# Performance work log

Hardware: AMD Instinct MI355X
Metric: run time of the kernel (lower is better)

Reference implementation:

```python
import jax, jax.numpy as jnp
import numpy as np

NUM_CLASSES = 80
ALPHA = 0.25
GAMMA = 2.0
CONF_T = 0.5
IOU_T = 0.5
N_ANCHORS = 6144


def _pairwise_iou(b):
    # b: [n,4] (x1,y1,x2,y2) -> [n,n] IoU matrix
    area = (b[:, 2] - b[:, 0]) * (b[:, 3] - b[:, 1])
    lt = jnp.maximum(b[:, None, :2], b[None, :, :2])
    rb = jnp.minimum(b[:, None, 2:], b[None, :, 2:])
    wh = jnp.clip(rb - lt, 0.0)
    inter = wh[..., 0] * wh[..., 1]
    return inter / (area[:, None] + area[None, :] - inter)


def _nms(boxes, scores, thr):
    # torchvision-style NMS: returns kept indices in decreasing-score order
    order = jnp.argsort(-scores)
    iou = _pairwise_iou(boxes[order])
    n = boxes.shape[0]
    ar = jnp.arange(n)
    def body(i, supp):
        return supp | ((iou[i] > thr) & (ar > i) & jnp.logical_not(supp[i]))
    supp = jax.lax.fori_loop(0, n, body, jnp.zeros(n, dtype=bool))
    kept_pos = jnp.where(~supp)[0]  # eager: concrete shapes
    return order[kept_pos]


def _make_boxes(tb, floc):
    # tb: [1,1,4] target box; floc: [Nf,2] filtered predicted locations
    # replicates loc_determined with T=1: (tx1*px, ty1*py, tx2*px, ty2*py)
    px, py = floc[:, 0], floc[:, 1]
    return jnp.stack([tb[0, 0, 0] * px, tb[0, 0, 1] * py,
                      tb[0, 0, 2] * px, tb[0, 0, 3] * py], axis=1)


def _smooth_l1_sum(pred, tgt):
    d = jnp.abs(pred - tgt)  # broadcasts [k,C,4] vs [1,1,4]
    return jnp.where(d < 1.0, 0.5 * d * d, d - 0.5).sum()


def setup_inputs() -> dict:
    key = jax.random.key(0)
    k1, k2, k3 = jax.random.split(key, 3)
    locations = jax.random.uniform(k1, (1, N_ANCHORS, 2), dtype=jnp.float32)
    confidences = jax.random.uniform(k2, (1, N_ANCHORS, NUM_CLASSES), dtype=jnp.float32)
    # valid target box (x1<x2, y1<y2) in [0,1]
    target_boxes = jnp.array([[[0.15, 0.2, 0.85, 0.9]]], dtype=jnp.float32)
    target_labels = jax.random.randint(k3, (1,), 0, NUM_CLASSES)
    return {"locations": locations, "confidences": confidences,
            "target_boxes": target_boxes, "target_labels": target_labels}


def reference(locations, confidences, target_boxes, target_labels):
    conf = confidences[0]                       # [N,C]
    scores_max = conf.max(axis=1)
    idx_f = jnp.where(scores_max > CONF_T)[0]   # eager boolean filter
    if idx_f.shape[0] == 0:
        return jnp.float32(0.001)
    floc = locations[0, idx_f, :]               # [Nf,2]
    fconf = conf[idx_f]                         # [Nf,C]
    boxes = _make_boxes(target_boxes, floc)     # [Nf,4] (pred_loc_final)
    score = fconf[:, 0]                         # class-0 score, as in original
    keep = _nms(boxes, score, IOU_T)            # kept indices
    if keep.shape[0] == 0:
        return jnp.float32(0.001)
    matched_loc = boxes[keep]                   # [M,4]
    matched_conf = fconf[keep]                  # [M,C]
    k = target_labels.shape[0]                  # = 1
    topv, topi = jax.lax.top_k(matched_conf.T, k)  # per-class top-k over dim 0
    topv, topi = topv.T, topi.T                 # [k,C]
    pred_bin = (topv[:, 0] > 0.5).astype(jnp.float32)  # [k]
    mloc = matched_loc[topi]                    # [k,C,4]
    loc_loss = _smooth_l1_sum(mloc, target_boxes)
    # F.cross_entropy with 1-D float input/target = probabilities mode, unbatched
    ce = -(target_labels.astype(jnp.float32) * jax.nn.log_softmax(pred_bin)).sum()
    focal = ALPHA * (1.0 - jnp.exp(-ce)) ** GAMMA * ce
    # original bug preserved: num_positives = sum of kept *indices*
    num_pos = keep.sum().astype(jnp.float32)
    return (loc_loss + focal) / num_pos
```

## Files before the change

### kernel.cpp

```cpp
#include <hip/hip_runtime.h>
#include <stdint.h>

#define N_ANCHORS 6144
#define NUM_CLASSES 80
#define NWORDS 96
#define NTILES 24
#define SCAN_B 32

__device__ unsigned long long g_mask[(size_t)N_ANCHORS * NWORDS + 64];
__device__ float4 g_sbox[N_ANCHORS];
__device__ int    g_rpart[NTILES][N_ANCHORS];
__device__ int    g_fpart[NTILES][N_ANCHORS];
__device__ int    g_sAnchor[N_ANCHORS];
__device__ int    g_sFi[N_ANCHORS];
__device__ int    g_keptPos[N_ANCHORS];
__device__ int    g_F, g_K, g_np, g_done;
__device__ float  g_loss;

__device__ __forceinline__ float rdlf(float v, int l) {
    return __int_as_float(__builtin_amdgcn_readlane(__float_as_int(v), l));
}

__device__ __forceinline__ float anchor_key(const float* __restrict__ conf, int i, bool& valid) {
    const float4* cp4 = (const float4*)(conf + (size_t)i * NUM_CLASSES);
    float4 v0 = cp4[0];
    float score = v0.x;
    float m = fmaxf(fmaxf(v0.x, v0.y), fmaxf(v0.z, v0.w));
    #pragma unroll
    for (int c = 1; c < NUM_CLASSES / 4; ++c) {
        float4 v = cp4[c];
        m = fmaxf(m, fmaxf(fmaxf(v.x, v.y), fmaxf(v.z, v.w)));
    }
    valid = m > 0.5f;
    return valid ? score : -1.0f;
}

__global__ void __launch_bounds__(256) k_rank(const float* __restrict__ conf) {
    __shared__ float skey[256];
    int y = blockIdx.y;
    int j0 = y * 256;
    bool vj;
    skey[threadIdx.x] = anchor_key(conf, j0 + threadIdx.x, vj);
    int i = blockIdx.x * 256 + threadIdx.x;
    bool vi;
    float ki = anchor_key(conf, i, vi);
    __syncthreads();
    int r = 0, f = 0;
    #pragma unroll 8
    for (int jj = 0; jj < 256; ++jj) {
        float kj = skey[jj];
        int j = j0 + jj;
        bool valid_j = kj >= 0.0f;
        r += (kj > ki) || (kj == ki && j < i && valid_j);
        f += (j < i) && valid_j;
    }
    g_rpart[y][i] = r;
    g_fpart[y][i] = f;
}

__global__ void __launch_bounds__(256) k_scatter(const float* __restrict__ loc,
                                                 const float* __restrict__ conf,
                                                 const float* __restrict__ tb) {
    int i = blockIdx.x * 256 + threadIdx.x;
    bool vi;
    float ki = anchor_key(conf, i, vi);
    (void)ki;
    int r = 0, f = 0;
    #pragma unroll
    for (int y = 0; y < NTILES; ++y) { r += g_rpart[y][i]; f += g_fpart[y][i]; }
    if (vi) {
        float px = loc[2 * i], py = loc[2 * i + 1];
        float4 b;
        b.x = __fmul_rn(tb[0], px);
        b.y = __fmul_rn(tb[1], py);
        b.z = __fmul_rn(tb[2], px);
        b.w = __fmul_rn(tb[3], py);
        g_sbox[r] = b;
        g_sAnchor[r] = i;
        g_sFi[r] = f;
    }
    if (i == N_ANCHORS - 1) g_F = f + (vi ? 1 : 0);
}

__global__ void __launch_bounds__(256) k_mask(void) {
    int wave = (blockIdx.x * 256 + threadIdx.x) >> 6;
    int lane = threadIdx.x & 63;
    if (wave >= N_ANCHORS) return;
    int i = wave;
    float4 bi = g_sbox[i];
    float areai = __fmul_rn(bi.z - bi.x, bi.w - bi.y);
    unsigned long long* row = g_mask + (size_t)i * NWORDS;
    for (int w = (i >> 6); w < NWORDS; ++w) {
        float4 bj = g_sbox[w * 64 + lane];
        float areaj = __fmul_rn(bj.z - bj.x, bj.w - bj.y);
        float lx = fmaxf(bi.x, bj.x), ly = fmaxf(bi.y, bj.y);
        float rx = fminf(bi.z, bj.z), ry = fminf(bi.w, bj.w);
        float iw = fmaxf(rx - lx, 0.0f), ih = fmaxf(ry - ly, 0.0f);
        float inter = __fmul_rn(iw, ih);
        float denom = __fsub_rn(__fadd_rn(areai, areaj), inter);
        float iou = __fdiv_rn(inter, denom);
        unsigned long long bits = __ballot(iou > 0.5f);
        if (lane == 0) row[w] = bits;
    }
}

__global__ void __launch_bounds__(64, 1) k_scan(void) {
    __shared__ int slots[SCAN_B];
    int lane = threadIdx.x;
    int F = g_F;
    if (lane == 0) { g_loss = 0.0f; g_np = 0; g_done = 0; }
    if (lane < SCAN_B) slots[lane] = 0;
    auto initw = [&](int w) -> unsigned long long {
        long long lo = (long long)w * 64, hi = lo + 64;
        if (F <= lo) return ~0ull;
        if (F >= hi) return 0ull;
        return (~0ull) << (F - lo);
    };
    unsigned long long remv0 = initw(lane);
    unsigned long long remv1 = (lane < 32) ? initw(64 + lane) : ~0ull;
    unsigned long long kept0 = 0, kept1 = 0;
    int lastPos = -1;

    while (true) {
        unsigned long long c0 = ~remv0;
        unsigned long long c1 = (lane < 32) ? ~remv1 : 0ull;
        {
            long long lo = (long long)lane << 6;
            if (lastPos >= lo + 63)      c0 = 0ull;
            else if (lastPos >= lo)      c0 &= (~0ull) << (int)(lastPos - lo + 1);
        }
        if (lane < 32) {
            long long lo = (long long)(64 + lane) << 6;
            if (lastPos >= lo + 63)      c1 = 0ull;
            else if (lastPos >= lo)      c1 &= (~0ull) << (int)(lastPos - lo + 1);
        }
        int n0 = __popcll(c0), n1 = __popcll(c1);
        int xp = (n0 << 16) | n1;
        for (int ofs = 1; ofs < 64; ofs <<= 1) {
            int y = __shfl_up(xp, ofs, 64);
            if (lane >= ofs) xp += y;
        }
        int lastxp = __builtin_amdgcn_readlane(xp, 63);
        int tot0 = lastxp >> 16, tot1 = lastxp & 0xffff;
        int total = tot0 + tot1;
        if (total == 0) break;
        int nb = (total < SCAN_B) ? total : SCAN_B;
        int off0 = (xp >> 16) - n0;
        int off1 = tot0 + ((xp & 0xffff) - n1);
        {
            unsigned long long wd = c0; int r = off0;
            while (wd && r < SCAN_B) { int b = __builtin_ctzll(wd); slots[r++] = lane * 64 + b; wd &= wd - 1; }
        }
        if (lane < 32) {
            unsigned long long wd = c1; int r = off1;
            while (wd && r < SCAN_B) { int b = __builtin_ctzll(wd); slots[r++] = (64 + lane) * 64 + b; wd &= wd - 1; }
        }
        __syncthreads();
        int myPos = slots[lane & 31];

        int Ps[SCAN_B];
        unsigned long long r0[SCAN_B], r1[SCAN_B];
        #pragma unroll
        for (int p = 0; p < SCAN_B; ++p) {
            Ps[p] = __builtin_amdgcn_readlane(myPos, p);
            const unsigned long long* rp = g_mask + (size_t)Ps[p] * NWORDS;
            r0[p] = rp[lane];
            r1[p] = rp[64 + lane];
        }

        float4 bj = g_sbox[myPos];
        float areaj = __fmul_rn(bj.z - bj.x, bj.w - bj.y);

        uint32_t conflict = 0;
        #pragma unroll
        for (int p = 0; p < SCAN_B; ++p) {
            float bix = rdlf(bj.x, p), biy = rdlf(bj.y, p), biz = rdlf(bj.z, p), biw = rdlf(bj.w, p);
            float areai = __fmul_rn(biz - bix, biw - biy);
            float lx = fmaxf(bix, bj.x), ly = fmaxf(biy, bj.y);
            float rx = fminf(biz, bj.z), ry = fminf(biw, bj.w);
            float iw = fmaxf(rx - lx, 0.0f), ih = fmaxf(ry - ly, 0.0f);
            float inter = __fmul_rn(iw, ih);
            float denom = __fsub_rn(__fadd_rn(areai, areaj), inter);
            float iou = __fdiv_rn(inter, denom);
            if (iou > 0.5f) conflict |= 1u << p;
        }
        conflict &= (nb >= 32) ? 0xffffffffu : ((1u << nb) - 1u);
        conflict &= (lane < nb) ? ((1u << lane) - 1u) : 0u;

        uint32_t keptm = 0;
        for (int p = 0; p < nb; ++p) {
            uint32_t cp = (uint32_t)__builtin_amdgcn_readlane((int)conflict, p);
            if ((cp & keptm) == 0u) keptm |= 1u << p;
        }

        #pragma unroll
        for (int p = 0; p < SCAN_B; ++p) {
            if ((keptm >> p) & 1u) {
                remv0 |= r0[p];
                remv1 |= r1[p];
                int P = Ps[p];
                int w = P >> 6, b = P & 63;
                if (w < 64) { if (lane == w) kept0 |= 1ull << b; }
                else        { if (lane == w - 64) kept1 |= 1ull << b; }
            }
        }
        lastPos = __builtin_amdgcn_readlane(myPos, nb - 1);
    }

    int c0 = __popcll(kept0);
    int c1 = (lane < 32) ? __popcll(kept1) : 0;
    int xp = (c0 << 16) | c1;
    for (int ofs = 1; ofs < 64; ofs <<= 1) {
        int y = __shfl_up(xp, ofs, 64);
        if (lane >= ofs) xp += y;
    }
    int lastxp = __builtin_amdgcn_readlane(xp, 63);
    int t0 = lastxp >> 16, t1 = lastxp & 0xffff;
    int off = (xp >> 16) - c0;
    unsigned long long wd = kept0;
    while (wd) { int b = __builtin_ctzll(wd); g_keptPos[off++] = lane * 64 + b; wd &= wd - 1; }
    off = t0 + ((xp & 0xffff) - c1);
    wd = kept1;
    while (wd) { int b = __builtin_ctzll(wd); g_keptPos[off++] = (64 + lane) * 64 + b; wd &= wd - 1; }
    if (lane == 0) g_K = t0 + t1;
}

__global__ void __launch_bounds__(64) k_loss(const float* __restrict__ conf, const float* __restrict__ tb,
                                             float* __restrict__ out) {
    int c = blockIdx.x;
    int lane = threadIdx.x;
    int K = g_K;
    float bv = -3.402823466e+38f;
    int bk = 0x7fffffff;
    int np = 0;
    for (int k = lane; k < K; k += 64) {
        int p = g_keptPos[k];
        int a = g_sAnchor[p];
        float v = conf[(size_t)a * NUM_CLASSES + c];
        if (v > bv || (v == bv && k < bk)) { bv = v; bk = k; }
        if (c == 0) np += g_sFi[p];
    }
    for (int ofs = 32; ofs > 0; ofs >>= 1) {
        float ov = __shfl_down(bv, ofs, 64);
        int ok = __shfl_down(bk, ofs, 64);
        if (ov > bv || (ov == bv && ok < bk)) { bv = ov; bk = ok; }
    }
    if (c == 0) {
        for (int ofs = 32; ofs > 0; ofs >>= 1) np += __shfl_down(np, ofs, 64);
        if (lane == 0) atomicExch(&g_np, np);
    }
    if (lane == 0) {
        if (K > 0) {
            float4 b = g_sbox[g_keptPos[bk]];
            float t0 = tb[0], t1 = tb[1], t2 = tb[2], t3 = tb[3];
            float l = 0.0f, d;
            d = fabsf(b.x - t0); l += (d < 1.0f) ? 0.5f * d * d : d - 0.5f;
            d = fabsf(b.y - t1); l += (d < 1.0f) ? 0.5f * d * d : d - 0.5f;
            d = fabsf(b.z - t2); l += (d < 1.0f) ? 0.5f * d * d : d - 0.5f;
            d = fabsf(b.w - t3); l += (d < 1.0f) ? 0.5f * d * d : d - 0.5f;
            atomicAdd(&g_loss, l);
        }
        __threadfence();
        int done = atomicAdd(&g_done, 1);
        if (done == NUM_CLASSES - 1) {
            float total = atomicAdd(&g_loss, 0.0f);
            int npv = atomicAdd(&g_np, 0);
            out[0] = (g_F == 0 || K == 0) ? 0.001f : total / (float)npv;
        }
    }
}

extern "C" void kernel_launch(void* const* d_in, const int* in_sizes, int n_in,
                              void* d_out, int out_size, void* d_ws, size_t ws_size,
                              hipStream_t stream) {
    const float* loc  = (const float*)d_in[0];
    const float* conf = (const float*)d_in[1];
    const float* tb   = (const float*)d_in[2];
    float* out = (float*)d_out;

    k_rank<<<dim3(NTILES, NTILES), 256, 0, stream>>>(conf);
    k_scatter<<<NTILES, 256, 0, stream>>>(loc, conf, tb);
    k_mask<<<(N_ANCHORS * 64) / 256, 256, 0, stream>>>();
    k_scan<<<1, 64, 0, stream>>>();
    k_loss<<<NUM_CLASSES, 64, 0, stream>>>(conf, tb, out);
}
```

Before: 167.9 us.

## Spread NMS scan mask-row loads across 16 waves with LDS removal bitmap

The serial NMS scan kernel now runs as a 1024-thread block instead of one wave. Wave 0 selects candidates and resolves conflicts within each batch, while waves 1-15 each load up to three suppression-mask rows and OR the kept ones into a shared-memory removal bitmap with atomics. This moves the 32 global row loads per batch off the single wave's critical path, at the cost of three block barriers and LDS atomics per iteration.

```diff
diff --git a/kernel.cpp b/kernel.cpp
--- a/kernel.cpp
+++ b/kernel.cpp
@@ -6,6 +6,7 @@
 #define NWORDS 96
 #define NTILES 24
 #define SCAN_B 32
+#define RPW 3
 
 __device__ unsigned long long g_mask[(size_t)N_ANCHORS * NWORDS + 64];
 __device__ float4 g_sbox[N_ANCHORS];
@@ -104,125 +105,158 @@
     }
 }
 
-__global__ void __launch_bounds__(64, 1) k_scan(void) {
+__global__ void __launch_bounds__(1024, 1) k_scan(void) {
+    __shared__ unsigned long long remv_lds[NWORDS];
     __shared__ int slots[SCAN_B];
-    int lane = threadIdx.x;
+    __shared__ int nbS, doneS;
+    __shared__ unsigned int keptmS;
+    int tid = threadIdx.x;
+    int wid = tid >> 6, lane = tid & 63;
     int F = g_F;
-    if (lane == 0) { g_loss = 0.0f; g_np = 0; g_done = 0; }
-    if (lane < SCAN_B) slots[lane] = 0;
     auto initw = [&](int w) -> unsigned long long {
         long long lo = (long long)w * 64, hi = lo + 64;
         if (F <= lo) return ~0ull;
         if (F >= hi) return 0ull;
         return (~0ull) << (F - lo);
     };
-    unsigned long long remv0 = initw(lane);
-    unsigned long long remv1 = (lane < 32) ? initw(64 + lane) : ~0ull;
+    if (tid < NWORDS) remv_lds[tid] = initw(tid);
+    if (tid < SCAN_B) slots[tid] = 0;
+    if (tid == 0) { g_loss = 0.0f; g_np = 0; g_done = 0; nbS = 0; doneS = 0; }
+    __syncthreads();
+
     unsigned long long kept0 = 0, kept1 = 0;
     int lastPos = -1;
 
-    while (true) {
-        unsigned long long c0 = ~remv0;
-        unsigned long long c1 = (lane < 32) ? ~remv1 : 0ull;
+    for (;;) {
+        if (wid == 0) {
+            unsigned long long c0 = ~remv_lds[lane];
+            unsigned long long c1 = (lane < 32) ? ~remv_lds[64 + lane] : 0ull;
+            {
+                long long lo = (long long)lane << 6;
+                if (lastPos >= lo + 63)      c0 = 0ull;
+                else if (lastPos >= lo)      c0 &= (~0ull) << (int)(lastPos - lo + 1);
+            }
+            if (lane < 32) {
+                long long lo = (long long)(64 + lane) << 6;
+                if (lastPos >= lo + 63)      c1 = 0ull;
+                else if (lastPos >= lo)      c1 &= (~0ull) << (int)(lastPos - lo + 1);
+            }
+            int n0 = __popcll(c0), n1 = __popcll(c1);
+            int xp = (n0 << 16) | n1;
+            for (int ofs = 1; ofs < 64; ofs <<= 1) {
+                int y = __shfl_up(xp, ofs, 64);
+                if (lane >= ofs) xp += y;
+            }
+            int lastxp = __builtin_amdgcn_readlane(xp, 63);
+            int tot0 = lastxp >> 16, tot1 = lastxp & 0xffff;
+            int total = tot0 + tot1;
+            int off0 = (xp >> 16) - n0;
+            int off1 = tot0 + ((xp & 0xffff) - n1);
+            {
+                unsigned long long wd = c0; int r = off0;
+                while (wd && r < SCAN_B) { int b = __builtin_ctzll(wd); slots[r++] = lane * 64 + b; wd &= wd - 1; }
+            }
+            if (lane < 32) {
+                unsigned long long wd = c1; int r = off1;
+                while (wd && r < SCAN_B) { int b = __builtin_ctzll(wd); slots[r++] = (64 + lane) * 64 + b; wd &= wd - 1; }
+            }
+            if (lane == 0) {
+                nbS = (total < SCAN_B) ? total : SCAN_B;
+                doneS = (total == 0);
+            }
+        }
+        __syncthreads();
+        if (doneS) break;
+        int nb = nbS;
+
+        unsigned long long a0[RPW], a1[RPW];
+        int rI[RPW];
+        #pragma unroll
+        for (int q = 0; q < RPW; ++q) {
+            rI[q] = RPW * (wid - 1) + q;
+            bool act = (wid >= 1) && (rI[q] < nb);
+            if (act) {
+                int P = slots[rI[q]];
+                const unsigned long long* rp = g_mask + (size_t)P * NWORDS;
+                a0[q] = rp[lane];
+                a1[q] = rp[64 + lane];
+            } else { a0[q] = 0ull; a1[q] = 0ull; }
+        }
+
+        if (wid == 0) {
+            int myPos = slots[lane & 31];
+            float4 bj = g_sbox[myPos];
+            float areaj = __fmul_rn(bj.z - bj.x, bj.w - bj.y);
+            uint32_t conflict = 0;
+            #pragma unroll
+            for (int p = 0; p < SCAN_B; ++p) {
+                float bix = rdlf(bj.x, p), biy = rdlf(bj.y, p), biz = rdlf(bj.z, p), biw = rdlf(bj.w, p);
+                float areai = __fmul_rn(biz - bix, biw - biy);
+                float lx = fmaxf(bix, bj.x), ly = fmaxf(biy, bj.y);
+                float rx = fminf(biz, bj.z), ry = fminf(biw, bj.w);
+                float iw = fmaxf(rx - lx, 0.0f), ih = fmaxf(ry - ly, 0.0f);
+                float inter = __fmul_rn(iw, ih);
+                float denom = __fsub_rn(__fadd_rn(areai, areaj), inter);
+                float iou = __fdiv_rn(inter, denom);
+                if (iou > 0.5f) conflict |= 1u << p;
+            }
+            conflict &= (nb >= 32) ? 0xffffffffu : ((1u << nb) - 1u);
+            conflict &= (lane < nb) ? ((1u << lane) - 1u) : 0u;
+            uint32_t keptm = 0;
+            for (int p = 0; p < nb; ++p) {
+                uint32_t cp = (uint32_t)__builtin_amdgcn_readlane((int)conflict, p);
+                if ((cp & keptm) == 0u) keptm |= 1u << p;
+            }
+            #pragma unroll
+            for (int p = 0; p < SCAN_B; ++p) {
+                if ((keptm >> p) & 1u) {
+                    int P = __builtin_amdgcn_readlane(myPos, p);
+                    int w = P >> 6, b = P & 63;
+                    if (w < 64) { if (lane == w) kept0 |= 1ull << b; }
+                    else        { if (lane == w - 64) kept1 |= 1ull << b; }
+                }
+            }
+            lastPos = __builtin_amdgcn_readlane(myPos, nb - 1);
+            if (lane == 0) keptmS = keptm;
+        }
+        __syncthreads();
+
         {
-            long long lo = (long long)lane << 6;
-            if (lastPos >= lo + 63)      c0 = 0ull;
-            else if (lastPos >= lo)      c0 &= (~0ull) << (int)(lastPos - lo + 1);
-        }
-        if (lane < 32) {
-            long long lo = (long long)(64 + lane) << 6;
-            if (lastPos >= lo + 63)      c1 = 0ull;
-            else if (lastPos >= lo)      c1 &= (~0ull) << (int)(lastPos - lo + 1);
-        }
-        int n0 = __popcll(c0), n1 = __popcll(c1);
-        int xp = (n0 << 16) | n1;
+            unsigned int km = keptmS;
+            unsigned int* rv32 = (unsigned int*)remv_lds;
+            #pragma unroll
+            for (int q = 0; q < RPW; ++q) {
+                if ((wid >= 1) && (rI[q] < nb) && ((km >> rI[q]) & 1u)) {
+                    atomicOr(&rv32[2 * lane],     (unsigned int)(a0[q] & 0xffffffffull));
+                    atomicOr(&rv32[2 * lane + 1], (unsigned int)(a0[q] >> 32));
+                    if (lane < 32) {
+                        atomicOr(&rv32[2 * (64 + lane)],     (unsigned int)(a1[q] & 0xffffffffull));
+                        atomicOr(&rv32[2 * (64 + lane) + 1], (unsigned int)(a1[q] >> 32));
+                    }
+                }
+            }
+        }
+        __syncthreads();
+    }
+
+    if (wid == 0) {
+        int c0 = __popcll(kept0);
+        int c1 = (lane < 32) ? __popcll(kept1) : 0;
+        int xp = (c0 << 16) | c1;
         for (int ofs = 1; ofs < 64; ofs <<= 1) {
             int y = __shfl_up(xp, ofs, 64);
             if (lane >= ofs) xp += y;
         }
         int lastxp = __builtin_amdgcn_readlane(xp, 63);
-        int tot0 = lastxp >> 16, tot1 = lastxp & 0xffff;
-        int total = tot0 + tot1;
-        if (total == 0) break;
-        int nb = (total < SCAN_B) ? total : SCAN_B;
-        int off0 = (xp >> 16) - n0;
-        int off1 = tot0 + ((xp & 0xffff) - n1);
-        {
-            unsigned long long wd = c0; int r = off0;
-            while (wd && r < SCAN_B) { int b = __builtin_ctzll(wd); slots[r++] = lane * 64 + b; wd &= wd - 1; }
-        }
-        if (lane < 32) {
-            unsigned long long wd = c1; int r = off1;
-            while (wd && r < SCAN_B) { int b = __builtin_ctzll(wd); slots[r++] = (64 + lane) * 64 + b; wd &= wd - 1; }
-        }
-        __syncthreads();
-        int myPos = slots[lane & 31];
-
-        int Ps[SCAN_B];
-        unsigned long long r0[SCAN_B], r1[SCAN_B];
-        #pragma unroll
-        for (int p = 0; p < SCAN_B; ++p) {
-            Ps[p] = __builtin_amdgcn_readlane(myPos, p);
-            const unsigned long long* rp = g_mask + (size_t)Ps[p] * NWORDS;
-            r0[p] = rp[lane];
-            r1[p] = rp[64 + lane];
-        }
-
-        float4 bj = g_sbox[myPos];
-        float areaj = __fmul_rn(bj.z - bj.x, bj.w - bj.y);
-
-        uint32_t conflict = 0;
-        #pragma unroll
-        for (int p = 0; p < SCAN_B; ++p) {
-            float bix = rdlf(bj.x, p), biy = rdlf(bj.y, p), biz = rdlf(bj.z, p), biw = rdlf(bj.w, p);
-            float areai = __fmul_rn(biz - bix, biw - biy);
-            float lx = fmaxf(bix, bj.x), ly = fmaxf(biy, bj.y);
-            float rx = fminf(biz, bj.z), ry = fminf(biw, bj.w);
-            float iw = fmaxf(rx - lx, 0.0f), ih = fmaxf(ry - ly, 0.0f);
-            float inter = __fmul_rn(iw, ih);
-            float denom = __fsub_rn(__fadd_rn(areai, areaj), inter);
-            float iou = __fdiv_rn(inter, denom);
-            if (iou > 0.5f) conflict |= 1u << p;
-        }
-        conflict &= (nb >= 32) ? 0xffffffffu : ((1u << nb) - 1u);
-        conflict &= (lane < nb) ? ((1u << lane) - 1u) : 0u;
-
-        uint32_t keptm = 0;
-        for (int p = 0; p < nb; ++p) {
-            uint32_t cp = (uint32_t)__builtin_amdgcn_readlane((int)conflict, p);
-            if ((cp & keptm) == 0u) keptm |= 1u << p;
-        }
-
-        #pragma unroll
-        for (int p = 0; p < SCAN_B; ++p) {
-            if ((keptm >> p) & 1u) {
-                remv0 |= r0[p];
-                remv1 |= r1[p];
-                int P = Ps[p];
-                int w = P >> 6, b = P & 63;
-                if (w < 64) { if (lane == w) kept0 |= 1ull << b; }
-                else        { if (lane == w - 64) kept1 |= 1ull << b; }
-            }
-        }
-        lastPos = __builtin_amdgcn_readlane(myPos, nb - 1);
-    }
-
-    int c0 = __popcll(kept0);
-    int c1 = (lane < 32) ? __popcll(kept1) : 0;
-    int xp = (c0 << 16) | c1;
-    for (int ofs = 1; ofs < 64; ofs <<= 1) {
-        int y = __shfl_up(xp, ofs, 64);
-        if (lane >= ofs) xp += y;
-    }
-    int lastxp = __builtin_amdgcn_readlane(xp, 63);
-    int t0 = lastxp >> 16, t1 = lastxp & 0xffff;
-    int off = (xp >> 16) - c0;
-    unsigned long long wd = kept0;
-    while (wd) { int b = __builtin_ctzll(wd); g_keptPos[off++] = lane * 64 + b; wd &= wd - 1; }
-    off = t0 + ((xp & 0xffff) - c1);
-    wd = kept1;
-    while (wd) { int b = __builtin_ctzll(wd); g_keptPos[off++] = (64 + lane) * 64 + b; wd &= wd - 1; }
-    if (lane == 0) g_K = t0 + t1;
+        int t0 = lastxp >> 16, t1 = lastxp & 0xffff;
+        int off = (xp >> 16) - c0;
+        unsigned long long wd = kept0;
+        while (wd) { int b = __builtin_ctzll(wd); g_keptPos[off++] = lane * 64 + b; wd &= wd - 1; }
+        off = t0 + ((xp & 0xffff) - c1);
+        wd = kept1;
+        while (wd) { int b = __builtin_ctzll(wd); g_keptPos[off++] = (64 + lane) * 64 + b; wd &= wd - 1; }
+        if (lane == 0) g_K = t0 + t1;
+    }
 }
 
 __global__ void __launch_bounds__(64) k_loss(const float* __restrict__ conf, const float* __restrict__ tb,
@@ -281,6 +315,6 @@
     k_rank<<<dim3(NTILES, NTILES), 256, 0, stream>>>(conf);
     k_scatter<<<NTILES, 256, 0, stream>>>(loc, conf, tb);
     k_mask<<<(N_ANCHORS * 64) / 256, 256, 0, stream>>>();
-    k_scan<<<1, 64, 0, stream>>>();
+    k_scan<<<1, 1024, 0, stream>>>();
     k_loss<<<NUM_CLASSES, 64, 0, stream>>>(conf, tb, out);
 }
```

After: 171.6 us. +2.2%, slower.
